# Kernel optimization log

Measured on AMD Instinct MI355X. Metric: run time of the kernel, lower is better.

Reference implementation:

```python
import jax, jax.numpy as jnp
import numpy as np

B = 8192      # batch size
D = 512       # feature dim == num_classes (centers is [C, C] in the original)
C = 512       # num_classes
MARGIN = 1.0


def setup_inputs() -> dict:
    key = jax.random.key(0)
    k1, k2, k3 = jax.random.split(key, 3)
    inputs = jax.random.normal(k1, (B, D), dtype=jnp.float32)
    targets = jax.random.randint(k2, (B,), 0, C)
    centers = jax.random.normal(k3, (C, D), dtype=jnp.float32)  # learned param
    return {"inputs": inputs, "targets": targets, "centers": centers}


def reference(inputs, targets, centers):
    # centers_batch[j] = centers[targets[j]]  (gather rows)
    cb = centers[targets]                                   # [B, D]
    # dist[i, j] = || inputs[i] - cb[j] ||_2, computed via the expanded form
    # (||a||^2 + ||b||^2 - 2 a.b) so we never materialize a [B, B, D] tensor.
    sq = ((inputs * inputs).sum(-1)[:, None]
          + (cb * cb).sum(-1)[None, :]
          - 2.0 * (inputs @ cb.T))                          # [B, B]
    dist = jnp.sqrt(jnp.clip(sq, 1e-12))                    # clamp(min=1e-12).sqrt()

    # mask[i, j] = (targets[i] == targets[j]); note original indexes dist[i][mask[i]]
    mask = targets[:, None] == targets[None, :]             # [B, B] bool
    dist_ap = jnp.max(jnp.where(mask, dist, -jnp.inf), axis=1)   # hardest positive per row
    dist_an = jnp.min(jnp.where(mask, jnp.inf, dist), axis=1)    # hardest negative per row

    # MarginRankingLoss(margin)(dist_an, dist_ap, y=1) = mean(relu(dist_ap - dist_an + margin))
    loss = jnp.mean(jnp.maximum(0.0, dist_ap - dist_an + MARGIN))
    prec = jnp.mean((dist_an > dist_ap).astype(jnp.float32))
    return loss, prec
```

## Files before the change

### kernel.cpp

```cpp
#include <hip/hip_runtime.h>
#include <hip/hip_bf16.h>

#define NB 8192
#define ND 512
#define NC 512
#define MARGIN_F 1.0f

typedef __attribute__((ext_vector_type(8))) short bf16x8;
typedef __attribute__((ext_vector_type(4))) float f32x4;

__device__ __forceinline__ unsigned fkey(float f) {
    unsigned u = __float_as_uint(f);
    unsigned mask = (u & 0x80000000u) ? 0xFFFFFFFFu : 0x80000000u;
    return u ^ mask;
}
__device__ __forceinline__ float finv(unsigned k) {
    unsigned mask = (k & 0x80000000u) ? 0x80000000u : 0xFFFFFFFFu;
    return __uint_as_float(k ^ mask);
}
__device__ __forceinline__ unsigned short f2bf(float f) {
    __hip_bfloat16 h = __float2bfloat16(f);
    return __builtin_bit_cast(unsigned short, h);
}

#define GLOAD_LDS16(g, l)                                                    \
    __builtin_amdgcn_global_load_lds(                                        \
        (const __attribute__((address_space(1))) void*)(g),                  \
        (__attribute__((address_space(3))) void*)(l), 16, 0, 0)

__global__ __launch_bounds__(256) void k0_prep(
    const float* __restrict__ inputs, const int* __restrict__ targets,
    const float* __restrict__ centers,
    unsigned short* __restrict__ inB, unsigned short* __restrict__ cenB,
    float* __restrict__ rsq, float* __restrict__ csq,
    unsigned* __restrict__ counts, unsigned* __restrict__ negmin)
{
    const int bid = blockIdx.x;
    const int tid = threadIdx.x;

    if (bid == 2176) {
        __shared__ unsigned hist[NC];
        for (int i = tid; i < NC; i += 256) hist[i] = 0u;
        __syncthreads();
        for (int i = tid; i < NB; i += 256) atomicAdd(&hist[targets[i]], 1u);
        __syncthreads();
        for (int i = tid; i < NC; i += 256) counts[i] = hist[i];
        return;
    }

    const int wave = tid >> 6, lane = tid & 63;
    const float* src;
    unsigned short* dst;
    float* sqdst;
    int row;
    bool is_input = (bid < 2048);
    if (is_input) {
        row   = bid * 4 + wave;
        src   = inputs + (size_t)row * ND;
        dst   = inB + (size_t)row * ND;
        sqdst = rsq + row;
    } else {
        row   = (bid - 2048) * 4 + wave;
        src   = centers + (size_t)row * ND;
        dst   = cenB + (size_t)row * ND;
        sqdst = csq + row;
    }

    float4 v1 = ((const float4*)src)[lane];
    float4 v2 = ((const float4*)src)[lane + 64];
    float s = v1.x*v1.x + v1.y*v1.y + v1.z*v1.z + v1.w*v1.w
            + v2.x*v2.x + v2.y*v2.y + v2.z*v2.z + v2.w*v2.w;

    ushort4 o1, o2;
    o1.x = f2bf(v1.x); o1.y = f2bf(v1.y); o1.z = f2bf(v1.z); o1.w = f2bf(v1.w);
    o2.x = f2bf(v2.x); o2.y = f2bf(v2.y); o2.z = f2bf(v2.z); o2.w = f2bf(v2.w);
    ((ushort4*)dst)[lane]      = o1;
    ((ushort4*)dst)[lane + 64] = o2;

    #pragma unroll
    for (int off = 32; off > 0; off >>= 1) s += __shfl_down(s, off);
    if (lane == 0) {
        *sqdst = s;
        if (is_input) negmin[row] = 0xFFFFFFFFu;
    }
}

__global__ __launch_bounds__(512) void k2_mfma(
    const unsigned short* __restrict__ Ain, const unsigned short* __restrict__ Cen,
    const int* __restrict__ targets, const unsigned* __restrict__ counts,
    const float* __restrict__ csq,
    unsigned* __restrict__ negmin, float* __restrict__ apval)
{
    __shared__ __align__(16) unsigned short As[128 * 32];
    __shared__ __align__(16) unsigned short Bs[128 * 32];
    __shared__ int      tgtL[128];
    __shared__ float    csqL[128];
    __shared__ unsigned cntL[128];

    const int tid  = threadIdx.x;
    const int w    = tid >> 6;
    const int lane = tid & 63;
    const int wm   = w >> 2;
    const int wn   = w & 3;
    const int qd   = lane >> 4;
    const int ln   = lane & 15;

    const int rbase = blockIdx.y * 128;
    const int cbase = blockIdx.x * 128;

    if (tid < 128) {
        tgtL[tid] = targets[rbase + tid];
        csqL[tid] = csq[cbase + tid];
        cntL[tid] = counts[cbase + tid];
    }

    const int srow  = w * 16 + (lane >> 2);
    const int scol  = (lane & 3) * 8;
    const unsigned short* gA = Ain + (size_t)(rbase + srow) * ND + scol;
    const unsigned short* gB = Cen + (size_t)(cbase + srow) * ND + scol;
    unsigned short* lA = &As[w * 16 * 32];
    unsigned short* lB = &Bs[w * 16 * 32];

    f32x4 acc[4][2] = {};

    for (int kb = 0; kb < ND; kb += 32) {
        __syncthreads();
        GLOAD_LDS16(gA + kb, lA);
        GLOAD_LDS16(gB + kb, lB);
        __syncthreads();

        bf16x8 a[4], b[2];
        #pragma unroll
        for (int i = 0; i < 4; ++i)
            a[i] = *(const bf16x8*)&As[(wm * 64 + i * 16 + ln) * 32 + qd * 8];
        #pragma unroll
        for (int j = 0; j < 2; ++j)
            b[j] = *(const bf16x8*)&Bs[(wn * 32 + j * 16 + ln) * 32 + qd * 8];
        #pragma unroll
        for (int i = 0; i < 4; ++i)
            #pragma unroll
            for (int j = 0; j < 2; ++j)
                acc[i][j] = __builtin_amdgcn_mfma_f32_16x16x32_bf16(a[i], b[j], acc[i][j], 0, 0, 0);
    }

    #pragma unroll
    for (int i = 0; i < 4; ++i) {
        #pragma unroll
        for (int r = 0; r < 4; ++r) {
            const int rlocal = wm * 64 + i * 16 + qd * 4 + r;
            const int grow   = rbase + rlocal;
            const int tr     = tgtL[rlocal];
            float m = 3.0e38f;
            #pragma unroll
            for (int j = 0; j < 2; ++j) {
                const int clocal = wn * 32 + j * 16 + ln;
                const float val = csqL[clocal] - 2.0f * acc[i][j][r];
                if (cbase + clocal == tr) {
                    apval[grow] = val;
                } else if (cntL[clocal] > 0u) {
                    m = fminf(m, val);
                }
            }
            #pragma unroll
            for (int off = 1; off < 16; off <<= 1)
                m = fminf(m, __shfl_xor(m, off));
            if (ln == 0)
                atomicMin(&negmin[grow], fkey(m));
        }
    }
}

__global__ __launch_bounds__(1024) void k3_final(
    const float* __restrict__ rsq, const unsigned* __restrict__ negmin,
    const float* __restrict__ apval, float* __restrict__ out)
{
    __shared__ float sl[1024];
    __shared__ float sp[1024];
    const int tid = threadIdx.x;
    float a = 0.0f, p = 0.0f;
    for (int r = tid; r < NB; r += 1024) {
        float s  = rsq[r];
        float an = sqrtf(fmaxf(s + finv(negmin[r]), 1e-12f));
        float ap = sqrtf(fmaxf(s + apval[r], 1e-12f));
        a += fmaxf(0.0f, ap - an + MARGIN_F);
        p += (an > ap) ? 1.0f : 0.0f;
    }
    sl[tid] = a; sp[tid] = p;
    __syncthreads();
    #pragma unroll
    for (int s = 512; s > 0; s >>= 1) {
        if (tid < s) { sl[tid] += sl[tid + s]; sp[tid] += sp[tid + s]; }
        __syncthreads();
    }
    if (tid == 0) {
        out[0] = sl[0] / (float)NB;
        out[1] = sp[0] / (float)NB;
    }
}

extern "C" void kernel_launch(void* const* d_in, const int* in_sizes, int n_in,
                              void* d_out, int out_size, void* d_ws, size_t ws_size,
                              hipStream_t stream) {
    const float* inputs  = (const float*)d_in[0];
    const int*   targets = (const int*)d_in[1];
    const float* centers = (const float*)d_in[2];
    float* out = (float*)d_out;

    char* w = (char*)d_ws;
    unsigned short* inB    = (unsigned short*)(w);
    unsigned short* cenB   = (unsigned short*)(w + 8388608);
    float*          rsq    = (float*)(w + 8912896);
    float*          csqv   = (float*)(w + 8945664);
    unsigned*       counts = (unsigned*)(w + 8947712);
    unsigned*       negmin = (unsigned*)(w + 8949760);
    float*          apval  = (float*)(w + 8982528);

    k0_prep<<<2177, 256, 0, stream>>>(inputs, targets, centers,
                                      inB, cenB, rsq, csqv, counts, negmin);
    k2_mfma<<<dim3(4, 64), 512, 0, stream>>>(inB, cenB, targets, counts, csqv,
                                             negmin, apval);
    k3_final<<<1, 1024, 0, stream>>>(rsq, negmin, apval, out);
}
```

Baseline: 96.72 us.

## Fuse input bf16 conversion and final reduction into the MFMA kernel

Measured after the change: 129.7 us. +34.1%, slower.

```diff
diff --git a/kernel.cpp b/kernel.cpp
--- a/kernel.cpp
+++ b/kernel.cpp
@@ -5,9 +5,11 @@
 #define ND 512
 #define NC 512
 #define MARGIN_F 1.0f
-
-typedef __attribute__((ext_vector_type(8))) short bf16x8;
-typedef __attribute__((ext_vector_type(4))) float f32x4;
+#define BIGF 3.0e38f
+
+typedef __attribute__((ext_vector_type(8))) short          bf16x8;
+typedef __attribute__((ext_vector_type(8))) unsigned short ushort8;
+typedef __attribute__((ext_vector_type(4))) float          f32x4;
 
 __device__ __forceinline__ unsigned fkey(float f) {
     unsigned u = __float_as_uint(f);
@@ -23,79 +25,60 @@
     return __builtin_bit_cast(unsigned short, h);
 }
 
-#define GLOAD_LDS16(g, l)                                                    \
-    __builtin_amdgcn_global_load_lds(                                        \
-        (const __attribute__((address_space(1))) void*)(g),                  \
-        (__attribute__((address_space(3))) void*)(l), 16, 0, 0)
-
 __global__ __launch_bounds__(256) void k0_prep(
-    const float* __restrict__ inputs, const int* __restrict__ targets,
-    const float* __restrict__ centers,
-    unsigned short* __restrict__ inB, unsigned short* __restrict__ cenB,
-    float* __restrict__ rsq, float* __restrict__ csq,
-    unsigned* __restrict__ counts, unsigned* __restrict__ negmin)
+    const float* __restrict__ centers, const int* __restrict__ targets,
+    unsigned short* __restrict__ cenB, float* __restrict__ csq,
+    unsigned* __restrict__ counts, unsigned* __restrict__ done)
 {
     const int bid = blockIdx.x;
     const int tid = threadIdx.x;
 
-    if (bid == 2176) {
+    if (bid == 128) {
         __shared__ unsigned hist[NC];
         for (int i = tid; i < NC; i += 256) hist[i] = 0u;
         __syncthreads();
         for (int i = tid; i < NB; i += 256) atomicAdd(&hist[targets[i]], 1u);
         __syncthreads();
         for (int i = tid; i < NC; i += 256) counts[i] = hist[i];
+        if (tid == 0) *done = 0u;
         return;
     }
 
     const int wave = tid >> 6, lane = tid & 63;
-    const float* src;
-    unsigned short* dst;
-    float* sqdst;
-    int row;
-    bool is_input = (bid < 2048);
-    if (is_input) {
-        row   = bid * 4 + wave;
-        src   = inputs + (size_t)row * ND;
-        dst   = inB + (size_t)row * ND;
-        sqdst = rsq + row;
-    } else {
-        row   = (bid - 2048) * 4 + wave;
-        src   = centers + (size_t)row * ND;
-        dst   = cenB + (size_t)row * ND;
-        sqdst = csq + row;
-    }
-
-    float4 v1 = ((const float4*)src)[lane];
-    float4 v2 = ((const float4*)src)[lane + 64];
+    const int c = bid * 4 + wave;
+    const float4* row = (const float4*)&centers[(size_t)c * ND];
+    float4 v1 = row[lane];
+    float4 v2 = row[lane + 64];
     float s = v1.x*v1.x + v1.y*v1.y + v1.z*v1.z + v1.w*v1.w
             + v2.x*v2.x + v2.y*v2.y + v2.z*v2.z + v2.w*v2.w;
 
     ushort4 o1, o2;
     o1.x = f2bf(v1.x); o1.y = f2bf(v1.y); o1.z = f2bf(v1.z); o1.w = f2bf(v1.w);
     o2.x = f2bf(v2.x); o2.y = f2bf(v2.y); o2.z = f2bf(v2.z); o2.w = f2bf(v2.w);
+    unsigned short* dst = cenB + (size_t)c * ND;
     ((ushort4*)dst)[lane]      = o1;
     ((ushort4*)dst)[lane + 64] = o2;
 
     #pragma unroll
     for (int off = 32; off > 0; off >>= 1) s += __shfl_down(s, off);
-    if (lane == 0) {
-        *sqdst = s;
-        if (is_input) negmin[row] = 0xFFFFFFFFu;
-    }
+    if (lane == 0) csq[c] = s;
 }
 
 __global__ __launch_bounds__(512) void k2_mfma(
-    const unsigned short* __restrict__ Ain, const unsigned short* __restrict__ Cen,
+    const float* __restrict__ inputs, const unsigned short* __restrict__ cenB,
     const int* __restrict__ targets, const unsigned* __restrict__ counts,
     const float* __restrict__ csq,
-    unsigned* __restrict__ negmin, float* __restrict__ apval)
+    float* __restrict__ partmin, float* __restrict__ apval,
+    float* __restrict__ rsq, unsigned* __restrict__ done,
+    float* __restrict__ out)
 {
-    __shared__ __align__(16) unsigned short As[128 * 32];
-    __shared__ __align__(16) unsigned short Bs[128 * 32];
+    __shared__ __align__(16) unsigned short As[128 * 72];
+    __shared__ __align__(16) unsigned short Bs[128 * 72];
     __shared__ int      tgtL[128];
     __shared__ float    csqL[128];
-    __shared__ unsigned cntL[128];
+    __shared__ unsigned ldsmin[128];
+    __shared__ float    red[16];
+    __shared__ int      lastFlag;
 
     const int tid  = threadIdx.x;
     const int w    = tid >> 6;
@@ -109,38 +92,73 @@
     const int cbase = blockIdx.x * 128;
 
     if (tid < 128) {
-        tgtL[tid] = targets[rbase + tid];
-        csqL[tid] = csq[cbase + tid];
-        cntL[tid] = counts[cbase + tid];
-    }
-
-    const int srow  = w * 16 + (lane >> 2);
-    const int scol  = (lane & 3) * 8;
-    const unsigned short* gA = Ain + (size_t)(rbase + srow) * ND + scol;
-    const unsigned short* gB = Cen + (size_t)(cbase + srow) * ND + scol;
-    unsigned short* lA = &As[w * 16 * 32];
-    unsigned short* lB = &Bs[w * 16 * 32];
+        tgtL[tid]   = targets[rbase + tid];
+        const int c = cbase + tid;
+        csqL[tid]   = (counts[c] > 0u) ? csq[c] : BIGF;
+        ldsmin[tid] = 0xFFFFFFFFu;
+    }
+
+    const int srow = tid >> 2;
+    const int scol = (tid & 3) * 16;
+    const float*          gA = inputs + (size_t)(rbase + srow) * ND + scol;
+    const unsigned short* gB = cenB   + (size_t)(cbase + srow) * ND + scol;
+    unsigned short* lA = &As[srow * 72 + scol];
+    unsigned short* lB = &Bs[srow * 72 + scol];
+
+    const bool do_rsq = (blockIdx.x == 0);
+    float rs = 0.0f;
 
     f32x4 acc[4][2] = {};
 
-    for (int kb = 0; kb < ND; kb += 32) {
-        __syncthreads();
-        GLOAD_LDS16(gA + kb, lA);
-        GLOAD_LDS16(gB + kb, lB);
-        __syncthreads();
-
-        bf16x8 a[4], b[2];
+    for (int kb = 0; kb < ND; kb += 64) {
+        float4  a0 = *(const float4*) (gA + kb + 0);
+        float4  a1 = *(const float4*) (gA + kb + 4);
+        float4  a2 = *(const float4*) (gA + kb + 8);
+        float4  a3 = *(const float4*) (gA + kb + 12);
+        ushort8 b0 = *(const ushort8*)(gB + kb + 0);
+        ushort8 b1 = *(const ushort8*)(gB + kb + 8);
+
+        if (do_rsq) {
+            rs += a0.x*a0.x + a0.y*a0.y + a0.z*a0.z + a0.w*a0.w;
+            rs += a1.x*a1.x + a1.y*a1.y + a1.z*a1.z + a1.w*a1.w;
+            rs += a2.x*a2.x + a2.y*a2.y + a2.z*a2.z + a2.w*a2.w;
+            rs += a3.x*a3.x + a3.y*a3.y + a3.z*a3.z + a3.w*a3.w;
+        }
+
+        ushort8 c0, c1;
+        c0[0]=f2bf(a0.x); c0[1]=f2bf(a0.y); c0[2]=f2bf(a0.z); c0[3]=f2bf(a0.w);
+        c0[4]=f2bf(a1.x); c0[5]=f2bf(a1.y); c0[6]=f2bf(a1.z); c0[7]=f2bf(a1.w);
+        c1[0]=f2bf(a2.x); c1[1]=f2bf(a2.y); c1[2]=f2bf(a2.z); c1[3]=f2bf(a2.w);
+        c1[4]=f2bf(a3.x); c1[5]=f2bf(a3.y); c1[6]=f2bf(a3.z); c1[7]=f2bf(a3.w);
+
+        __syncthreads();
+        *(ushort8*)lA       = c0;
+        *(ushort8*)(lA + 8) = c1;
+        *(ushort8*)lB       = b0;
+        *(ushort8*)(lB + 8) = b1;
+        __syncthreads();
+
         #pragma unroll
-        for (int i = 0; i < 4; ++i)
-            a[i] = *(const bf16x8*)&As[(wm * 64 + i * 16 + ln) * 32 + qd * 8];
-        #pragma unroll
-        for (int j = 0; j < 2; ++j)
-            b[j] = *(const bf16x8*)&Bs[(wn * 32 + j * 16 + ln) * 32 + qd * 8];
-        #pragma unroll
-        for (int i = 0; i < 4; ++i)
+        for (int ks = 0; ks < 2; ++ks) {
+            bf16x8 a[4], b[2];
+            #pragma unroll
+            for (int i = 0; i < 4; ++i)
+                a[i] = *(const bf16x8*)&As[(wm*64 + i*16 + ln)*72 + ks*32 + qd*8];
             #pragma unroll
             for (int j = 0; j < 2; ++j)
-                acc[i][j] = __builtin_amdgcn_mfma_f32_16x16x32_bf16(a[i], b[j], acc[i][j], 0, 0, 0);
+                b[j] = *(const bf16x8*)&Bs[(wn*32 + j*16 + ln)*72 + ks*32 + qd*8];
+            #pragma unroll
+            for (int i = 0; i < 4; ++i)
+                #pragma unroll
+                for (int j = 0; j < 2; ++j)
+                    acc[i][j] = __builtin_amdgcn_mfma_f32_16x16x32_bf16(a[i], b[j], acc[i][j], 0, 0, 0);
+        }
+    }
+
+    if (do_rsq) {
+        rs += __shfl_xor(rs, 1);
+        rs += __shfl_xor(rs, 2);
+        if ((tid & 3) == 0) rsq[rbase + srow] = rs;
     }
 
     #pragma unroll
@@ -150,51 +168,59 @@
             const int rlocal = wm * 64 + i * 16 + qd * 4 + r;
             const int grow   = rbase + rlocal;
             const int tr     = tgtL[rlocal];
-            float m = 3.0e38f;
+            float m = BIGF;
             #pragma unroll
             for (int j = 0; j < 2; ++j) {
                 const int clocal = wn * 32 + j * 16 + ln;
                 const float val = csqL[clocal] - 2.0f * acc[i][j][r];
                 if (cbase + clocal == tr) {
                     apval[grow] = val;
-                } else if (cntL[clocal] > 0u) {
+                } else {
                     m = fminf(m, val);
                 }
             }
             #pragma unroll
             for (int off = 1; off < 16; off <<= 1)
                 m = fminf(m, __shfl_xor(m, off));
-            if (ln == 0)
-                atomicMin(&negmin[grow], fkey(m));
+            if (ln == 0) atomicMin(&ldsmin[rlocal], fkey(m));
         }
     }
-}
-
-__global__ __launch_bounds__(1024) void k3_final(
-    const float* __restrict__ rsq, const unsigned* __restrict__ negmin,
-    const float* __restrict__ apval, float* __restrict__ out)
-{
-    __shared__ float sl[1024];
-    __shared__ float sp[1024];
-    const int tid = threadIdx.x;
-    float a = 0.0f, p = 0.0f;
-    for (int r = tid; r < NB; r += 1024) {
-        float s  = rsq[r];
-        float an = sqrtf(fmaxf(s + finv(negmin[r]), 1e-12f));
-        float ap = sqrtf(fmaxf(s + apval[r], 1e-12f));
-        a += fmaxf(0.0f, ap - an + MARGIN_F);
-        p += (an > ap) ? 1.0f : 0.0f;
-    }
-    sl[tid] = a; sp[tid] = p;
     __syncthreads();
+    if (tid < 128)
+        partmin[(size_t)blockIdx.x * NB + rbase + tid] = finv(ldsmin[tid]);
+
+    __threadfence();
+    if (tid == 0) {
+        unsigned old = atomicAdd(done, 1u);
+        lastFlag = (old == 255u) ? 1 : 0;
+    }
+    __syncthreads();
+    if (!lastFlag) return;
+    __threadfence();
+
+    float la = 0.0f, lp = 0.0f;
+    for (int rr = tid; rr < NB; rr += 512) {
+        float m = fminf(fminf(partmin[rr],        partmin[NB + rr]),
+                        fminf(partmin[2*NB + rr], partmin[3*NB + rr]));
+        float s  = rsq[rr];
+        float an = sqrtf(fmaxf(s + m,         1e-12f));
+        float ap = sqrtf(fmaxf(s + apval[rr], 1e-12f));
+        la += fmaxf(0.0f, ap - an + MARGIN_F);
+        lp += (an > ap) ? 1.0f : 0.0f;
+    }
     #pragma unroll
-    for (int s = 512; s > 0; s >>= 1) {
-        if (tid < s) { sl[tid] += sl[tid + s]; sp[tid] += sp[tid + s]; }
-        __syncthreads();
-    }
+    for (int off = 32; off > 0; off >>= 1) {
+        la += __shfl_down(la, off);
+        lp += __shfl_down(lp, off);
+    }
+    if (lane == 0) { red[w] = la; red[8 + w] = lp; }
+    __syncthreads();
     if (tid == 0) {
-        out[0] = sl[0] / (float)NB;
-        out[1] = sp[0] / (float)NB;
+        float A = 0.0f, P = 0.0f;
+        #pragma unroll
+        for (int i = 0; i < 8; ++i) { A += red[i]; P += red[8 + i]; }
+        out[0] = A / (float)NB;
+        out[1] = P / (float)NB;
     }
 }
 
@@ -206,18 +232,16 @@
     const float* centers = (const float*)d_in[2];
     float* out = (float*)d_out;
 
-    char* w = (char*)d_ws;
-    unsigned short* inB    = (unsigned short*)(w);
-    unsigned short* cenB   = (unsigned short*)(w + 8388608);
-    float*          rsq    = (float*)(w + 8912896);
-    float*          csqv   = (float*)(w + 8945664);
-    unsigned*       counts = (unsigned*)(w + 8947712);
-    unsigned*       negmin = (unsigned*)(w + 8949760);
-    float*          apval  = (float*)(w + 8982528);
-
-    k0_prep<<<2177, 256, 0, stream>>>(inputs, targets, centers,
-                                      inB, cenB, rsq, csqv, counts, negmin);
-    k2_mfma<<<dim3(4, 64), 512, 0, stream>>>(inB, cenB, targets, counts, csqv,
-                                             negmin, apval);
-    k3_final<<<1, 1024, 0, stream>>>(rsq, negmin, apval, out);
-}
+    char* wp = (char*)d_ws;
+    unsigned short* cenB    = (unsigned short*)(wp);
+    float*          csqv    = (float*)(wp + 524288);
+    unsigned*       counts  = (unsigned*)(wp + 526336);
+    float*          rsq     = (float*)(wp + 528384);
+    float*          apval   = (float*)(wp + 561152);
+    float*          partmin = (float*)(wp + 593920);
+    unsigned*       done    = (unsigned*)(wp + 724992);
+
+    k0_prep<<<129, 256, 0, stream>>>(centers, targets, cenB, csqv, counts, done);
+    k2_mfma<<<dim3(4, 64), 512, 0, stream>>>(inputs, cenB, targets, counts, csqv,
+                                             partmin, apval, rsq, done, out);
+}
```

## Fuse final reduction into GEMM kernel via last-block counter and retile to 512 blocks

Applied to the files above, without the earlier changes.

Measured after the change: 129.2 us. +33.6%, slower.

```diff
diff --git a/kernel.cpp b/kernel.cpp
--- a/kernel.cpp
+++ b/kernel.cpp
@@ -5,9 +5,10 @@
 #define ND 512
 #define NC 512
 #define MARGIN_F 1.0f
-
-typedef __attribute__((ext_vector_type(8))) short bf16x8;
-typedef __attribute__((ext_vector_type(4))) float f32x4;
+#define BIGF 3.0e38f
+
+typedef __attribute__((ext_vector_type(8))) short          bf16x8;
+typedef __attribute__((ext_vector_type(4))) float          f32x4;
 
 __device__ __forceinline__ unsigned fkey(float f) {
     unsigned u = __float_as_uint(f);
@@ -33,7 +34,8 @@
     const float* __restrict__ centers,
     unsigned short* __restrict__ inB, unsigned short* __restrict__ cenB,
     float* __restrict__ rsq, float* __restrict__ csq,
-    unsigned* __restrict__ counts, unsigned* __restrict__ negmin)
+    unsigned* __restrict__ counts, unsigned* __restrict__ negmin,
+    unsigned* __restrict__ done)
 {
     const int bid = blockIdx.x;
     const int tid = threadIdx.x;
@@ -45,6 +47,7 @@
         for (int i = tid; i < NB; i += 256) atomicAdd(&hist[targets[i]], 1u);
         __syncthreads();
         for (int i = tid; i < NC; i += 256) counts[i] = hist[i];
+        if (tid == 0) *done = 0u;
         return;
     }
 
@@ -85,48 +88,57 @@
     }
 }
 
-__global__ __launch_bounds__(512) void k2_mfma(
-    const unsigned short* __restrict__ Ain, const unsigned short* __restrict__ Cen,
+__global__ __launch_bounds__(256) void k2_mfma(
+    const unsigned short* __restrict__ Ain, const unsigned short* __restrict__ cenB,
     const int* __restrict__ targets, const unsigned* __restrict__ counts,
     const float* __restrict__ csq,
-    unsigned* __restrict__ negmin, float* __restrict__ apval)
+    unsigned* __restrict__ negmin, float* __restrict__ apval,
+    const float* __restrict__ rsq, unsigned* __restrict__ done,
+    float* __restrict__ out)
 {
     __shared__ __align__(16) unsigned short As[128 * 32];
-    __shared__ __align__(16) unsigned short Bs[128 * 32];
+    __shared__ __align__(16) unsigned short Bs[64 * 32];
     __shared__ int      tgtL[128];
-    __shared__ float    csqL[128];
-    __shared__ unsigned cntL[128];
+    __shared__ float    csqL[64];
+    __shared__ unsigned ldsmin[128];
+    __shared__ float    red[8];
+    __shared__ int      lastFlag;
 
     const int tid  = threadIdx.x;
     const int w    = tid >> 6;
     const int lane = tid & 63;
-    const int wm   = w >> 2;
-    const int wn   = w & 3;
+    const int wm   = w >> 1;
+    const int wn   = w & 1;
     const int qd   = lane >> 4;
     const int ln   = lane & 15;
 
-    const int rbase = blockIdx.y * 128;
-    const int cbase = blockIdx.x * 128;
-
-    if (tid < 128) {
-        tgtL[tid] = targets[rbase + tid];
-        csqL[tid] = csq[cbase + tid];
-        cntL[tid] = counts[cbase + tid];
-    }
-
-    const int srow  = w * 16 + (lane >> 2);
+    const int bid   = blockIdx.x;
+    const int rbase = (bid & 63) * 128;
+    const int cbase = (bid >> 6) * 64;
+
+    if (tid < 128) { tgtL[tid] = targets[rbase + tid]; ldsmin[tid] = 0xFFFFFFFFu; }
+    if (tid < 64) {
+        const int c = cbase + tid;
+        csqL[tid] = (counts[c] > 0u) ? csq[c] : BIGF;
+    }
+
+    const int arow0 = w * 32 + (lane >> 2);
+    const int brow  = w * 16 + (lane >> 2);
     const int scol  = (lane & 3) * 8;
-    const unsigned short* gA = Ain + (size_t)(rbase + srow) * ND + scol;
-    const unsigned short* gB = Cen + (size_t)(cbase + srow) * ND + scol;
-    unsigned short* lA = &As[w * 16 * 32];
-    unsigned short* lB = &Bs[w * 16 * 32];
+    const unsigned short* gA0 = Ain  + (size_t)(rbase + arow0)      * ND + scol;
+    const unsigned short* gA1 = Ain  + (size_t)(rbase + arow0 + 16) * ND + scol;
+    const unsigned short* gB  = cenB + (size_t)(cbase + brow)       * ND + scol;
+    unsigned short* lA0 = &As[(w * 32)      * 32];
+    unsigned short* lA1 = &As[(w * 32 + 16) * 32];
+    unsigned short* lB  = &Bs[(w * 16)      * 32];
 
     f32x4 acc[4][2] = {};
 
     for (int kb = 0; kb < ND; kb += 32) {
         __syncthreads();
-        GLOAD_LDS16(gA + kb, lA);
-        GLOAD_LDS16(gB + kb, lB);
+        GLOAD_LDS16(gA0 + kb, lA0);
+        GLOAD_LDS16(gA1 + kb, lA1);
+        GLOAD_LDS16(gB  + kb, lB);
         __syncthreads();
 
         bf16x8 a[4], b[2];
@@ -150,51 +162,59 @@
             const int rlocal = wm * 64 + i * 16 + qd * 4 + r;
             const int grow   = rbase + rlocal;
             const int tr     = tgtL[rlocal];
-            float m = 3.0e38f;
+            float m = BIGF;
             #pragma unroll
             for (int j = 0; j < 2; ++j) {
                 const int clocal = wn * 32 + j * 16 + ln;
                 const float val = csqL[clocal] - 2.0f * acc[i][j][r];
                 if (cbase + clocal == tr) {
                     apval[grow] = val;
-                } else if (cntL[clocal] > 0u) {
+                } else {
                     m = fminf(m, val);
                 }
             }
             #pragma unroll
             for (int off = 1; off < 16; off <<= 1)
                 m = fminf(m, __shfl_xor(m, off));
-            if (ln == 0)
-                atomicMin(&negmin[grow], fkey(m));
+            if (ln == 0) atomicMin(&ldsmin[rlocal], fkey(m));
         }
     }
-}
-
-__global__ __launch_bounds__(1024) void k3_final(
-    const float* __restrict__ rsq, const unsigned* __restrict__ negmin,
-    const float* __restrict__ apval, float* __restrict__ out)
-{
-    __shared__ float sl[1024];
-    __shared__ float sp[1024];
-    const int tid = threadIdx.x;
-    float a = 0.0f, p = 0.0f;
-    for (int r = tid; r < NB; r += 1024) {
-        float s  = rsq[r];
-        float an = sqrtf(fmaxf(s + finv(negmin[r]), 1e-12f));
-        float ap = sqrtf(fmaxf(s + apval[r], 1e-12f));
-        a += fmaxf(0.0f, ap - an + MARGIN_F);
-        p += (an > ap) ? 1.0f : 0.0f;
-    }
-    sl[tid] = a; sp[tid] = p;
     __syncthreads();
+    if (tid < 128) {
+        unsigned v = ldsmin[tid];
+        if (v != 0xFFFFFFFFu) atomicMin(&negmin[rbase + tid], v);
+    }
+
+    __threadfence();
+    if (tid == 0) {
+        unsigned old = atomicAdd(done, 1u);
+        lastFlag = (old == 511u) ? 1 : 0;
+    }
+    __syncthreads();
+    if (!lastFlag) return;
+    __threadfence();
+
+    float la = 0.0f, lp = 0.0f;
+    for (int rr = tid; rr < NB; rr += 256) {
+        float s  = rsq[rr];
+        float an = sqrtf(fmaxf(s + finv(negmin[rr]), 1e-12f));
+        float ap = sqrtf(fmaxf(s + apval[rr],        1e-12f));
+        la += fmaxf(0.0f, ap - an + MARGIN_F);
+        lp += (an > ap) ? 1.0f : 0.0f;
+    }
     #pragma unroll
-    for (int s = 512; s > 0; s >>= 1) {
-        if (tid < s) { sl[tid] += sl[tid + s]; sp[tid] += sp[tid + s]; }
-        __syncthreads();
-    }
+    for (int off = 32; off > 0; off >>= 1) {
+        la += __shfl_down(la, off);
+        lp += __shfl_down(lp, off);
+    }
+    if (lane == 0) { red[w] = la; red[4 + w] = lp; }
+    __syncthreads();
     if (tid == 0) {
-        out[0] = sl[0] / (float)NB;
-        out[1] = sp[0] / (float)NB;
+        float A = 0.0f, P = 0.0f;
+        #pragma unroll
+        for (int i = 0; i < 4; ++i) { A += red[i]; P += red[4 + i]; }
+        out[0] = A / (float)NB;
+        out[1] = P / (float)NB;
     }
 }
 
@@ -206,18 +226,18 @@
     const float* centers = (const float*)d_in[2];
     float* out = (float*)d_out;
 
-    char* w = (char*)d_ws;
-    unsigned short* inB    = (unsigned short*)(w);
-    unsigned short* cenB   = (unsigned short*)(w + 8388608);
-    float*          rsq    = (float*)(w + 8912896);
-    float*          csqv   = (float*)(w + 8945664);
-    unsigned*       counts = (unsigned*)(w + 8947712);
-    unsigned*       negmin = (unsigned*)(w + 8949760);
-    float*          apval  = (float*)(w + 8982528);
+    char* wp = (char*)d_ws;
+    unsigned short* inB    = (unsigned short*)(wp);
+    unsigned short* cenB   = (unsigned short*)(wp + 8388608);
+    float*          rsq    = (float*)(wp + 8912896);
+    float*          csqv   = (float*)(wp + 8945664);
+    unsigned*       counts = (unsigned*)(wp + 8947712);
+    unsigned*       negmin = (unsigned*)(wp + 8949760);
+    float*          apval  = (float*)(wp + 8982528);
+    unsigned*       done   = (unsigned*)(wp + 9015296);
 
     k0_prep<<<2177, 256, 0, stream>>>(inputs, targets, centers,
-                                      inB, cenB, rsq, csqv, counts, negmin);
-    k2_mfma<<<dim3(4, 64), 512, 0, stream>>>(inB, cenB, targets, counts, csqv,
-                                             negmin, apval);
-    k3_final<<<1, 1024, 0, stream>>>(rsq, negmin, apval, out);
-}
+                                      inB, cenB, rsq, csqv, counts, negmin, done);
+    k2_mfma<<<512, 256, 0, stream>>>(inB, cenB, targets, counts, csqv,
+                                     negmin, apval, rsq, done, out);
+}
```
